# Optimization experiments

Measured on AMD Instinct MI355X. Metric: run time of the kernel, lower is better.

Reference implementation:

```python
import jax, jax.numpy as jnp
import numpy as np

B, S, D = 16, 1024, 768
H = 12
DH = D // H  # 64

def setup_inputs() -> dict:
    key = jax.random.key(0)
    ks = jax.random.split(key, 7)
    scale = 1.0 / np.sqrt(D)
    return {
        "hidden_states": jax.random.normal(ks[0], (B, S, D), dtype=jnp.float32),
        "Wq": jax.random.normal(ks[1], (D, D), dtype=jnp.float32) * scale,
        "bq": jnp.zeros((D,), dtype=jnp.float32),
        "Wk": jax.random.normal(ks[2], (D, D), dtype=jnp.float32) * scale,
        "bk": jnp.zeros((D,), dtype=jnp.float32),
        "Wv": jax.random.normal(ks[3], (D, D), dtype=jnp.float32) * scale,
        "bv": jnp.zeros((D,), dtype=jnp.float32),
    }

def reference(hidden_states, Wq, bq, Wk, bk, Wv, bv):
    # QKV projections: [B,S,D] -> [B,S,H,DH] -> [B,H,S,DH]
    def proj(W, b):
        y = hidden_states @ W.T + b
        return y.reshape(B, S, H, DH).transpose(0, 2, 1, 3)
    q = proj(Wq, bq)
    k = proj(Wk, bk)
    v = proj(Wv, bv)
    # attention scores [B,H,S,S], scaled by sqrt(d_head)
    scores = jnp.einsum('bhqd,bhkd->bhqk', q, k) / jnp.sqrt(jnp.float32(DH))
    probs = jax.nn.softmax(scores, axis=-1)
    # dropout prob = 0.0 (eval) -> identity
    ctx = jnp.einsum('bhqk,bhkd->bhqd', probs, v)
    ctx = ctx.transpose(0, 2, 1, 3).reshape(B, S, D)
    return ctx
```

## Files before the change

kernel.cpp:

```cpp
#include <hip/hip_runtime.h>
#include <hip/hip_bf16.h>

typedef __attribute__((ext_vector_type(8))) short short8;
typedef __attribute__((ext_vector_type(4))) float float4v;
typedef __attribute__((ext_vector_type(2))) unsigned int uint2v;

#define MFMA_BF16 __builtin_amdgcn_mfma_f32_16x16x32_bf16

__device__ __forceinline__ unsigned short f2b(float f) {
  union { float f; unsigned u; } v; v.f = f;
  unsigned r = v.u + 0x7FFFu + ((v.u >> 16) & 1u);
  return (unsigned short)(r >> 16);
}

__device__ __forceinline__ unsigned pk2(float x, float y) {
  float2 v; v.x = x; v.y = y;
  __hip_bfloat162 h = __float22bfloat162_rn(v);
  union { __hip_bfloat162 h; unsigned u; } c; c.h = h;
  return c.u;
}

__device__ __forceinline__ void gld16(const unsigned short* g, unsigned short* l) {
  __builtin_amdgcn_global_load_lds(
      (const __attribute__((address_space(1))) unsigned int*)g,
      (__attribute__((address_space(3))) unsigned int*)l, 16, 0, 0);
}

__device__ __forceinline__ int swa(int r, int k) {
  return (r << 6) + ((((k >> 3) ^ r ^ (r >> 3)) & 7) << 3) + (k & 7);
}

__global__ __launch_bounds__(256) void cast_f32_bf16(const float* __restrict__ src,
                                                     unsigned short* __restrict__ dst,
                                                     int n4) {
  int i = blockIdx.x * 256 + threadIdx.x;
  if (i >= n4) return;
  float4 f = ((const float4*)src)[i];
  uint2 o;
  o.x = pk2(f.x, f.y);
  o.y = pk2(f.z, f.w);
  ((uint2*)dst)[i] = o;
}

__global__ __launch_bounds__(256) void cast_w3(const float* __restrict__ s0,
                                               const float* __restrict__ s1,
                                               const float* __restrict__ s2,
                                               unsigned short* __restrict__ dst) {
  const int z = blockIdx.y;
  const float* src = (z == 0) ? s0 : (z == 1 ? s1 : s2);
  int i = blockIdx.x * 256 + threadIdx.x;
  float4 f = ((const float4*)src)[i];
  uint2 o;
  o.x = pk2(f.x, f.y);
  o.y = pk2(f.z, f.w);
  ((uint2*)(dst + (size_t)z * 589824))[i] = o;
}

__global__ __launch_bounds__(256) void qkv_gemm(
    const unsigned short* __restrict__ X, const unsigned short* __restrict__ Wall,
    const float* __restrict__ b0, const float* __restrict__ b1, const float* __restrict__ b2,
    unsigned short* __restrict__ O0, unsigned short* __restrict__ O1, unsigned short* __restrict__ OVT) {
  __shared__ __align__(16) unsigned short Sh[16384];
  unsigned short* As = Sh;
  unsigned short* Bs = Sh + 8192;
  const int z = blockIdx.z;
  const unsigned short* W = Wall + (size_t)z * 589824;
  const float* bias = (z == 0) ? b0 : (z == 1 ? b1 : b2);
  const int m0 = blockIdx.x * 128, n0 = blockIdx.y * 128;
  const int t = threadIdx.x, w = t >> 6, l = t & 63, qd = l >> 4, col = l & 15;
  const int wm = (w & 1) * 64, wn = (w >> 1) * 64;

  float4v acc[4][4];
#pragma unroll
  for (int i = 0; i < 4; ++i)
#pragma unroll
    for (int j = 0; j < 4; ++j) acc[i][j] = (float4v)0.0f;

  const unsigned short* Xp = X + (size_t)m0 * 768;
  const unsigned short* Wp = W + (size_t)n0 * 768;

  for (int k0 = 0; k0 < 768; k0 += 64) {
#pragma unroll
    for (int p = 0; p < 4; ++p) {
      const int c = p * 256 + t;
      const int row = c >> 3;
      const int cc = (c ^ row ^ (row >> 3)) & 7;
      gld16(&Xp[(size_t)row * 768 + k0 + cc * 8], &As[c * 8]);
      gld16(&Wp[(size_t)row * 768 + k0 + cc * 8], &Bs[c * 8]);
    }
    __syncthreads();
#pragma unroll
    for (int ks = 0; ks < 2; ++ks) {
      short8 af[4], bf[4];
#pragma unroll
      for (int mi = 0; mi < 4; ++mi)
        af[mi] = *(const short8*)&As[swa(wm + mi * 16 + col, ks * 32 + qd * 8)];
#pragma unroll
      for (int ni = 0; ni < 4; ++ni)
        bf[ni] = *(const short8*)&Bs[swa(wn + ni * 16 + col, ks * 32 + qd * 8)];
#pragma unroll
      for (int mi = 0; mi < 4; ++mi)
#pragma unroll
        for (int ni = 0; ni < 4; ++ni)
          acc[mi][ni] = MFMA_BF16(af[mi], bf[ni], acc[mi][ni], 0, 0, 0);
    }
    __syncthreads();
  }

  if (z < 2) {
    unsigned short* O = (z == 0) ? O0 : O1;
    const float osc = (z == 0) ? 0.18033688f : 1.0f;
#pragma unroll
    for (int ni = 0; ni < 4; ++ni) {
      const int n = n0 + wn + ni * 16 + col;
      const float bb = bias[n];
#pragma unroll
      for (int mi = 0; mi < 4; ++mi)
#pragma unroll
        for (int r = 0; r < 4; ++r) {
          const int m = m0 + wm + mi * 16 + qd * 4 + r;
          O[(size_t)m * 768 + n] = f2b((acc[mi][ni][r] + bb) * osc);
        }
    }
  } else {
#pragma unroll
    for (int ni = 0; ni < 4; ++ni) {
      const int nl = wn + ni * 16 + col;
      const float bb = bias[n0 + nl];
#pragma unroll
      for (int mi = 0; mi < 4; ++mi) {
        const int ml = wm + mi * 16 + qd * 4;
        ushort4 o;
        o.x = f2b(acc[mi][ni][0] + bb);
        o.y = f2b(acc[mi][ni][1] + bb);
        o.z = f2b(acc[mi][ni][2] + bb);
        o.w = f2b(acc[mi][ni][3] + bb);
        *(ushort4*)&Sh[(nl << 7) + ((((ml >> 3) ^ nl) & 15) << 3) + (ml & 7)] = o;
      }
    }
    __syncthreads();
    const int nl = t >> 1, mh = (t & 1) * 64;
    const int n = n0 + nl, hh = n >> 6, dd = n & 63;
    unsigned short* dstp =
        &OVT[(((size_t)(m0 >> 10) * 12 + hh) * 64 + dd) * 1024 + (m0 & 1023) + mh];
#pragma unroll
    for (int j = 0; j < 8; ++j) {
      const int mc = (mh >> 3) + j;
      uint4 vv = *(const uint4*)&Sh[(nl << 7) + (((mc ^ nl) & 15) << 3)];
      *(uint4*)&dstp[j * 8] = vv;
    }
  }
}

__global__ __launch_bounds__(256) void attn(
    const unsigned short* __restrict__ Q, const unsigned short* __restrict__ K,
    const unsigned short* __restrict__ VT, float* __restrict__ O) {
  __shared__ __align__(16) unsigned short Ks0[4096];
  __shared__ __align__(16) unsigned short Ks1[4096];
  __shared__ __align__(16) unsigned short Vt0[4096];
  __shared__ __align__(16) unsigned short Vt1[4096];

  const int g = blockIdx.x;
  const int orig = (g & 7) * 192 + (g >> 3);
  const int qt = orig & 7;
  const int hb = orig >> 3;
  const int b = hb / 12;
  const int h = hb - b * 12;

  const int t = threadIdx.x, w = t >> 6, l = t & 63, qd = l >> 4, col = l & 15;
  const size_t bh = (size_t)b * 786432 + (size_t)h * 64;
  const unsigned short* Kb = K + bh;
  const unsigned short* VTb = VT + ((size_t)(b * 12 + h)) * 65536;

  short8 qf[2][2];
  {
    const unsigned short* Qg = Q + bh + (size_t)(qt * 128 + w * 32) * 768;
#pragma unroll
    for (int mi = 0; mi < 2; ++mi)
#pragma unroll
      for (int ks = 0; ks < 2; ++ks)
        qf[mi][ks] =
            *(const short8*)&Qg[(size_t)(mi * 16 + col) * 768 + ks * 32 + qd * 8];
  }

  const int c0 = t, c1 = 256 + t;
  const int r0 = c0 >> 3, cc0 = (c0 ^ r0 ^ (r0 >> 3)) & 7;
  const int r1 = c1 >> 3, cc1 = (c1 ^ r1 ^ (r1 >> 3)) & 7;

#define STAGE_K(ktile, dst)                                             \
  do {                                                                  \
    const unsigned short* Kg_ = Kb + (size_t)(ktile)*49152;             \
    gld16(&Kg_[(size_t)r0 * 768 + cc0 * 8], &dst[c0 * 8]);              \
    gld16(&Kg_[(size_t)r1 * 768 + cc1 * 8], &dst[c1 * 8]);              \
  } while (0)

#define STAGE_V(ktile, dst)                                             \
  do {                                                                  \
    const unsigned short* Vg_ = VTb + (ktile)*64;                       \
    gld16(&Vg_[(size_t)r0 * 1024 + cc0 * 8], &dst[c0 * 8]);             \
    gld16(&Vg_[(size_t)r1 * 1024 + cc1 * 8], &dst[c1 * 8]);             \
  } while (0)

  STAGE_K(0, Ks0);
  STAGE_V(0, Vt0);

  float4v acc[2][4];
  float4v accl[2];
#pragma unroll
  for (int mi = 0; mi < 2; ++mi) {
    accl[mi] = (float4v)0.0f;
#pragma unroll
    for (int dt = 0; dt < 4; ++dt) acc[mi][dt] = (float4v)0.0f;
  }

  short8 ones;
#pragma unroll
  for (int j = 0; j < 8; ++j) ones[j] = (short)0x3F80;

  __syncthreads();

#define ATTN_ITER(kt, KsR, VtR, KsW, VtW)                                 \
  do {                                                                    \
    if ((kt) < 15) {                                                      \
      STAGE_K((kt) + 1, KsW);                                             \
      STAGE_V((kt) + 1, VtW);                                             \
    }                                                                     \
    short8 kf[2][4];                                                      \
    _Pragma("unroll") for (int ks = 0; ks < 2; ++ks)                      \
        _Pragma("unroll") for (int ni = 0; ni < 4; ++ni)                  \
        kf[ks][ni] =                                                      \
        *(const short8*)&KsR[swa(ni * 16 + col, ks * 32 + qd * 8)];       \
    float4v sT[2][4];                                                     \
    _Pragma("unroll") for (int mi = 0; mi < 2; ++mi)                      \
        _Pragma("unroll") for (int ni = 0; ni < 4; ++ni)                  \
        sT[mi][ni] = (float4v)0.0f;                                       \
    _Pragma("unroll") for (int ks = 0; ks < 2; ++ks)                      \
        _Pragma("unroll") for (int ni = 0; ni < 4; ++ni) {                \
      sT[0][ni] = MFMA_BF16(kf[ks][ni], qf[0][ks], sT[0][ni], 0, 0, 0);   \
      sT[1][ni] = MFMA_BF16(kf[ks][ni], qf[1][ks], sT[1][ni], 0, 0, 0);   \
    }                                                                     \
    _Pragma("unroll") for (int s = 0; s < 2; ++s) {                       \
      short8 pf[2];                                                       \
      _Pragma("unroll") for (int mi = 0; mi < 2; ++mi) {                  \
        float4v sa = sT[mi][s * 2 + 0];                                   \
        float4v sb = sT[mi][s * 2 + 1];                                   \
        unsigned A0 = pk2(__builtin_amdgcn_exp2f(sa[0]),                  \
                          __builtin_amdgcn_exp2f(sa[1]));                 \
        unsigned A1 = pk2(__builtin_amdgcn_exp2f(sa[2]),                  \
                          __builtin_amdgcn_exp2f(sa[3]));                 \
        unsigned B0 = pk2(__builtin_amdgcn_exp2f(sb[0]),                  \
                          __builtin_amdgcn_exp2f(sb[1]));                 \
        unsigned B1 = pk2(__builtin_amdgcn_exp2f(sb[2]),                  \
                          __builtin_amdgcn_exp2f(sb[3]));                 \
         \
        uint2v x0 = __builtin_amdgcn_permlane32_swap(A0, B0, false, false);   \
        uint2v x1 = __builtin_amdgcn_permlane32_swap(A1, B1, false, false);   \
        uint2v y02 = __builtin_amdgcn_permlane16_swap(x0[0], x0[1], false, false); \
        uint2v y13 = __builtin_amdgcn_permlane16_swap(x1[0], x1[1], false, false); \
        union { unsigned u[4]; short8 v; } pu;                            \
        pu.u[0] = y02[0]; pu.u[1] = y13[0];                               \
        pu.u[2] = y02[1]; pu.u[3] = y13[1];                               \
        pf[mi] = pu.v;                                                    \
      }                                                                   \
      const int kk = s * 32 + qd * 8;                                     \
      _Pragma("unroll") for (int dt = 0; dt < 4; ++dt) {                  \
        short8 vf = *(const short8*)&VtR[swa(dt * 16 + col, kk)];         \
        acc[0][dt] = MFMA_BF16(vf, pf[0], acc[0][dt], 0, 0, 0);           \
        acc[1][dt] = MFMA_BF16(vf, pf[1], acc[1][dt], 0, 0, 0);           \
      }                                                                   \
      accl[0] = MFMA_BF16(ones, pf[0], accl[0], 0, 0, 0);                 \
      accl[1] = MFMA_BF16(ones, pf[1], accl[1], 0, 0, 0);                 \
    }                                                                     \
    __syncthreads();                                                      \
  } while (0)

  for (int kt2 = 0; kt2 < 16; kt2 += 2) {
    ATTN_ITER(kt2, Ks0, Vt0, Ks1, Vt1);
    ATTN_ITER(kt2 + 1, Ks1, Vt1, Ks0, Vt0);
  }

  float* Og = O + (size_t)(b * 1024 + qt * 128) * 768 + h * 64;
#pragma unroll
  for (int mi = 0; mi < 2; ++mi) {
    const float rl = 1.0f / accl[mi][0];
    const int q = w * 32 + mi * 16 + col;
#pragma unroll
    for (int dt = 0; dt < 4; ++dt) {
      float4 o;
      o.x = acc[mi][dt][0] * rl;
      o.y = acc[mi][dt][1] * rl;
      o.z = acc[mi][dt][2] * rl;
      o.w = acc[mi][dt][3] * rl;
      *(float4*)&Og[(size_t)q * 768 + dt * 16 + qd * 4] = o;
    }
  }
#undef STAGE_K
#undef STAGE_V
#undef ATTN_ITER
}

extern "C" void kernel_launch(void* const* d_in, const int* in_sizes, int n_in,
                              void* d_out, int out_size, void* d_ws, size_t ws_size,
                              hipStream_t stream) {
  const float* hs = (const float*)d_in[0];
  const float* Wq = (const float*)d_in[1];
  const float* bq = (const float*)d_in[2];
  const float* Wk = (const float*)d_in[3];
  const float* bk = (const float*)d_in[4];
  const float* Wv = (const float*)d_in[5];
  const float* bv = (const float*)d_in[6];
  float* out = (float*)d_out;
  char* ws = (char*)d_ws;

  unsigned short* Xb = (unsigned short*)ws;
  unsigned short* Wb = (unsigned short*)(ws + 25165824);
  unsigned short* Qb = (unsigned short*)(ws + 28704768);
  unsigned short* Kb = (unsigned short*)(ws + 53870592);
  unsigned short* Vb = (unsigned short*)(ws + 79036416);

  cast_f32_bf16<<<12288, 256, 0, stream>>>(hs, Xb, 3145728);
  cast_w3<<<dim3(576, 3), 256, 0, stream>>>(Wq, Wk, Wv, Wb);

  qkv_gemm<<<dim3(128, 6, 3), 256, 0, stream>>>(Xb, Wb, bq, bk, bv, Qb, Kb, Vb);

  attn<<<dim3(1536), 256, 0, stream>>>(Qb, Kb, Vb, out);
}
```

Measured before the change: 273.1 us.

## Pipeline QKV GEMM with triple-buffered LDS, larger tiles, and merged cast kernels

Merges the two fp32-to-bf16 cast kernels into one launch. Rewrites the QKV projection GEMM to use 512-thread blocks with 256x128 tiles over a flattened 1D grid that treats the three weight matrices as one 2304-wide N dimension, with a swizzled block order. The K loop becomes a three-stage global_load_lds pipeline using explicit vmcnt waits and raw barriers, and MFMA issue priority is raised. The aim is to hide global-load latency and cut per-iteration sync stalls, at the cost of 144KB of dynamic LDS per block, which limits occupancy to one block per CU.

```diff
diff --git a/kernel.cpp b/kernel.cpp
--- a/kernel.cpp
+++ b/kernel.cpp
@@ -30,11 +30,25 @@
   return (r << 6) + ((((k >> 3) ^ r ^ (r >> 3)) & 7) << 3) + (k & 7);
 }
 
-__global__ __launch_bounds__(256) void cast_f32_bf16(const float* __restrict__ src,
-                                                     unsigned short* __restrict__ dst,
-                                                     int n4) {
-  int i = blockIdx.x * 256 + threadIdx.x;
-  if (i >= n4) return;
+__global__ __launch_bounds__(256) void cast_all(
+    const float* __restrict__ hs, const float* __restrict__ Wq,
+    const float* __restrict__ Wk, const float* __restrict__ Wv,
+    unsigned short* __restrict__ Xb, unsigned short* __restrict__ Wb) {
+  const int blk = blockIdx.x;
+  const float* src;
+  unsigned short* dst;
+  int i;
+  if (blk < 12288) {
+    i = blk * 256 + threadIdx.x;
+    src = hs;
+    dst = Xb;
+  } else {
+    const int x = blk - 12288;
+    const int z = x / 576;
+    i = (x - z * 576) * 256 + threadIdx.x;
+    src = (z == 0) ? Wq : (z == 1 ? Wk : Wv);
+    dst = Wb + (size_t)z * 589824;
+  }
   float4 f = ((const float4*)src)[i];
   uint2 o;
   o.x = pk2(f.x, f.y);
@@ -42,33 +56,51 @@
   ((uint2*)dst)[i] = o;
 }
 
-__global__ __launch_bounds__(256) void cast_w3(const float* __restrict__ s0,
-                                               const float* __restrict__ s1,
-                                               const float* __restrict__ s2,
-                                               unsigned short* __restrict__ dst) {
-  const int z = blockIdx.y;
-  const float* src = (z == 0) ? s0 : (z == 1 ? s1 : s2);
-  int i = blockIdx.x * 256 + threadIdx.x;
-  float4 f = ((const float4*)src)[i];
-  uint2 o;
-  o.x = pk2(f.x, f.y);
-  o.y = pk2(f.z, f.w);
-  ((uint2*)(dst + (size_t)z * 589824))[i] = o;
-}
-
-__global__ __launch_bounds__(256) void qkv_gemm(
+__global__ __launch_bounds__(512) void qkv_gemm(
     const unsigned short* __restrict__ X, const unsigned short* __restrict__ Wall,
     const float* __restrict__ b0, const float* __restrict__ b1, const float* __restrict__ b2,
     unsigned short* __restrict__ O0, unsigned short* __restrict__ O1, unsigned short* __restrict__ OVT) {
-  __shared__ __align__(16) unsigned short Sh[16384];
-  unsigned short* As = Sh;
-  unsigned short* Bs = Sh + 8192;
-  const int z = blockIdx.z;
-  const unsigned short* W = Wall + (size_t)z * 589824;
-  const float* bias = (z == 0) ? b0 : (z == 1 ? b1 : b2);
-  const int m0 = blockIdx.x * 128, n0 = blockIdx.y * 128;
+  extern __shared__ __align__(16) unsigned short LDS[];
+
+  const int g = blockIdx.x;
+  const int orig = (g & 7) * 144 + (g >> 3);
+  const int mblk = orig / 18;
+  const int nblk = orig - mblk * 18;
+  const int m0 = mblk * 256, n0p = nblk * 128;
+
   const int t = threadIdx.x, w = t >> 6, l = t & 63, qd = l >> 4, col = l & 15;
-  const int wm = (w & 1) * 64, wn = (w >> 1) * 64;
+  const int wm64 = (w & 3) * 64, wn64 = (w >> 2) * 64;
+  const int qd8 = qd * 8;
+
+  const int cA0 = t, cA1 = 512 + t, cA2 = 1024 + t, cA3 = 1536 + t;
+  const int rA0 = cA0 >> 3, rA1 = cA1 >> 3, rA2 = cA2 >> 3, rA3 = cA3 >> 3;
+  const int pA0 = (cA0 ^ rA0 ^ (rA0 >> 3)) & 7, pA1 = (cA1 ^ rA1 ^ (rA1 >> 3)) & 7;
+  const int pA2 = (cA2 ^ rA2 ^ (rA2 >> 3)) & 7, pA3 = (cA3 ^ rA3 ^ (rA3 >> 3)) & 7;
+  const int cB0 = t, cB1 = 512 + t;
+  const int rB0 = cB0 >> 3, rB1 = cB1 >> 3;
+  const int pB0 = (cB0 ^ rB0 ^ (rB0 >> 3)) & 7, pB1 = (cB1 ^ rB1 ^ (rB1 >> 3)) & 7;
+
+  const unsigned short* Xa0 = X + (size_t)(m0 + rA0) * 768 + pA0 * 8;
+  const unsigned short* Xa1 = X + (size_t)(m0 + rA1) * 768 + pA1 * 8;
+  const unsigned short* Xa2 = X + (size_t)(m0 + rA2) * 768 + pA2 * 8;
+  const unsigned short* Xa3 = X + (size_t)(m0 + rA3) * 768 + pA3 * 8;
+  const unsigned short* Wb0 = Wall + (size_t)(n0p + rB0) * 768 + pB0 * 8;
+  const unsigned short* Wb1 = Wall + (size_t)(n0p + rB1) * 768 + pB1 * 8;
+  const int dA0 = cA0 * 8, dA1 = cA1 * 8, dA2 = cA2 * 8, dA3 = cA3 * 8;
+  const int dB0 = cB0 * 8, dB1 = cB1 * 8;
+
+#define STAGE(kt, sb)                                         \
+  do {                                                        \
+    unsigned short* SA_ = LDS + (sb)*24576;                   \
+    unsigned short* SB_ = SA_ + 16384;                        \
+    const int kk_ = (kt)*64;                                  \
+    gld16(Xa0 + kk_, SA_ + dA0);                              \
+    gld16(Xa1 + kk_, SA_ + dA1);                              \
+    gld16(Xa2 + kk_, SA_ + dA2);                              \
+    gld16(Xa3 + kk_, SA_ + dA3);                              \
+    gld16(Wb0 + kk_, SB_ + dB0);                              \
+    gld16(Wb1 + kk_, SB_ + dB1);                              \
+  } while (0)
 
   float4v acc[4][4];
 #pragma unroll
@@ -76,80 +108,105 @@
 #pragma unroll
     for (int j = 0; j < 4; ++j) acc[i][j] = (float4v)0.0f;
 
-  const unsigned short* Xp = X + (size_t)m0 * 768;
-  const unsigned short* Wp = W + (size_t)n0 * 768;
-
-  for (int k0 = 0; k0 < 768; k0 += 64) {
-#pragma unroll
-    for (int p = 0; p < 4; ++p) {
-      const int c = p * 256 + t;
-      const int row = c >> 3;
-      const int cc = (c ^ row ^ (row >> 3)) & 7;
-      gld16(&Xp[(size_t)row * 768 + k0 + cc * 8], &As[c * 8]);
-      gld16(&Wp[(size_t)row * 768 + k0 + cc * 8], &Bs[c * 8]);
-    }
-    __syncthreads();
-#pragma unroll
-    for (int ks = 0; ks < 2; ++ks) {
-      short8 af[4], bf[4];
+#define COMPUTE(cur)                                                          \
+  do {                                                                        \
+    const unsigned short* Ar_ = LDS + (cur)*24576;                            \
+    const unsigned short* Br_ = Ar_ + 16384;                                  \
+    _Pragma("unroll") for (int ks = 0; ks < 2; ++ks) {                        \
+      short8 af[4], bf[4];                                                    \
+      _Pragma("unroll") for (int mi = 0; mi < 4; ++mi)                        \
+          af[mi] = *(const short8*)&Ar_[swa(wm64 + mi * 16 + col,             \
+                                            ks * 32 + qd8)];                  \
+      _Pragma("unroll") for (int ni = 0; ni < 4; ++ni)                        \
+          bf[ni] = *(const short8*)&Br_[swa(wn64 + ni * 16 + col,             \
+                                            ks * 32 + qd8)];                  \
+      __builtin_amdgcn_s_setprio(1);                                          \
+      _Pragma("unroll") for (int mi = 0; mi < 4; ++mi)                        \
+          _Pragma("unroll") for (int ni = 0; ni < 4; ++ni)                    \
+          acc[mi][ni] = MFMA_BF16(af[mi], bf[ni], acc[mi][ni], 0, 0, 0);      \
+      __builtin_amdgcn_s_setprio(0);                                          \
+    }                                                                         \
+  } while (0)
+
+  STAGE(0, 0);
+  STAGE(1, 1);
+  asm volatile("s_waitcnt vmcnt(6)" ::: "memory");
+  __builtin_amdgcn_s_barrier();
+  __builtin_amdgcn_sched_barrier(0);
+
+  int cur = 0;
+#pragma unroll 1
+  for (int kt = 0; kt < 10; ++kt) {
+    const int sb = (cur == 0) ? 2 : cur - 1;
+    STAGE(kt + 2, sb);
+    COMPUTE(cur);
+    asm volatile("s_waitcnt vmcnt(6)" ::: "memory");
+    __builtin_amdgcn_s_barrier();
+    __builtin_amdgcn_sched_barrier(0);
+    cur = (cur == 2) ? 0 : cur + 1;
+  }
+  COMPUTE(cur);
+  asm volatile("s_waitcnt vmcnt(0)" ::: "memory");
+  __builtin_amdgcn_s_barrier();
+  __builtin_amdgcn_sched_barrier(0);
+  cur = (cur == 2) ? 0 : cur + 1;
+  COMPUTE(cur);
+
+  const int zz = n0p / 768;
+  const int nbase = n0p - zz * 768;
+
+  if (zz < 2) {
+    unsigned short* O = (zz == 0) ? O0 : O1;
+    const float* bias = (zz == 0) ? b0 : b1;
+    const float osc = (zz == 0) ? 0.18033688f : 1.0f;
+#pragma unroll
+    for (int ni = 0; ni < 4; ++ni) {
+      const int n = nbase + wn64 + ni * 16 + col;
+      const float bb = bias[n];
 #pragma unroll
       for (int mi = 0; mi < 4; ++mi)
-        af[mi] = *(const short8*)&As[swa(wm + mi * 16 + col, ks * 32 + qd * 8)];
-#pragma unroll
-      for (int ni = 0; ni < 4; ++ni)
-        bf[ni] = *(const short8*)&Bs[swa(wn + ni * 16 + col, ks * 32 + qd * 8)];
-#pragma unroll
-      for (int mi = 0; mi < 4; ++mi)
-#pragma unroll
-        for (int ni = 0; ni < 4; ++ni)
-          acc[mi][ni] = MFMA_BF16(af[mi], bf[ni], acc[mi][ni], 0, 0, 0);
-    }
-    __syncthreads();
-  }
-
-  if (z < 2) {
-    unsigned short* O = (z == 0) ? O0 : O1;
-    const float osc = (z == 0) ? 0.18033688f : 1.0f;
-#pragma unroll
-    for (int ni = 0; ni < 4; ++ni) {
-      const int n = n0 + wn + ni * 16 + col;
-      const float bb = bias[n];
-#pragma unroll
-      for (int mi = 0; mi < 4; ++mi)
 #pragma unroll
         for (int r = 0; r < 4; ++r) {
-          const int m = m0 + wm + mi * 16 + qd * 4 + r;
+          const int m = m0 + wm64 + mi * 16 + qd * 4 + r;
           O[(size_t)m * 768 + n] = f2b((acc[mi][ni][r] + bb) * osc);
         }
     }
   } else {
+    __syncthreads();
+    unsigned short* T = LDS;
 #pragma unroll
     for (int ni = 0; ni < 4; ++ni) {
-      const int nl = wn + ni * 16 + col;
-      const float bb = bias[n0 + nl];
+      const int nl = wn64 + ni * 16 + col;
+      const float bb = b2[nbase + nl];
 #pragma unroll
       for (int mi = 0; mi < 4; ++mi) {
-        const int ml = wm + mi * 16 + qd * 4;
+        const int ml = wm64 + mi * 16 + qd * 4;
+        const int mc = ml >> 3;
         ushort4 o;
         o.x = f2b(acc[mi][ni][0] + bb);
         o.y = f2b(acc[mi][ni][1] + bb);
         o.z = f2b(acc[mi][ni][2] + bb);
         o.w = f2b(acc[mi][ni][3] + bb);
-        *(ushort4*)&Sh[(nl << 7) + ((((ml >> 3) ^ nl) & 15) << 3) + (ml & 7)] = o;
+        *(ushort4*)&T[(nl << 8) + (((mc ^ (nl & 31)) & 31) << 3) + (ml & 7)] = o;
       }
     }
     __syncthreads();
-    const int nl = t >> 1, mh = (t & 1) * 64;
-    const int n = n0 + nl, hh = n >> 6, dd = n & 63;
+    const int nl2 = t >> 2;
+    const int seg = t & 3;
+    const int nglob = nbase + nl2;
+    const int hh = nglob >> 6, dd = nglob & 63;
+    const int bb2 = m0 >> 10;
     unsigned short* dstp =
-        &OVT[(((size_t)(m0 >> 10) * 12 + hh) * 64 + dd) * 1024 + (m0 & 1023) + mh];
+        &OVT[(((size_t)bb2 * 12 + hh) * 64 + dd) * 1024 + (m0 & 1023) + seg * 64];
 #pragma unroll
     for (int j = 0; j < 8; ++j) {
-      const int mc = (mh >> 3) + j;
-      uint4 vv = *(const uint4*)&Sh[(nl << 7) + (((mc ^ nl) & 15) << 3)];
+      const int mc = seg * 8 + j;
+      uint4 vv = *(const uint4*)&T[(nl2 << 8) + (((mc ^ (nl2 & 31)) & 31) << 3)];
       *(uint4*)&dstp[j * 8] = vv;
     }
   }
+#undef STAGE
+#undef COMPUTE
 }
 
 __global__ __launch_bounds__(256) void attn(
@@ -252,7 +309,6 @@
                           __builtin_amdgcn_exp2f(sb[1]));                 \
         unsigned B1 = pk2(__builtin_amdgcn_exp2f(sb[2]),                  \
                           __builtin_amdgcn_exp2f(sb[3]));                 \
-         \
         uint2v x0 = __builtin_amdgcn_permlane32_swap(A0, B0, false, false);   \
         uint2v x1 = __builtin_amdgcn_permlane32_swap(A1, B1, false, false);   \
         uint2v y02 = __builtin_amdgcn_permlane16_swap(x0[0], x0[1], false, false); \
@@ -318,10 +374,16 @@
   unsigned short* Kb = (unsigned short*)(ws + 53870592);
   unsigned short* Vb = (unsigned short*)(ws + 79036416);
 
-  cast_f32_bf16<<<12288, 256, 0, stream>>>(hs, Xb, 3145728);
-  cast_w3<<<dim3(576, 3), 256, 0, stream>>>(Wq, Wk, Wv, Wb);
-
-  qkv_gemm<<<dim3(128, 6, 3), 256, 0, stream>>>(Xb, Wb, bq, bk, bv, Qb, Kb, Vb);
+  static bool attr_set = false;
+  if (!attr_set) {
+    hipFuncSetAttribute((const void*)qkv_gemm,
+                        hipFuncAttributeMaxDynamicSharedMemorySize, 147456);
+    attr_set = true;
+  }
+
+  cast_all<<<14016, 256, 0, stream>>>(hs, Wq, Wk, Wv, Xb, Wb);
+
+  qkv_gemm<<<dim3(1152), 512, 147456, stream>>>(Xb, Wb, bq, bk, bv, Qb, Kb, Vb);
 
   attn<<<dim3(1536), 256, 0, stream>>>(Qb, Kb, Vb, out);
 }
```

After: 259.7 us. 1.05x faster.
